# Kernel optimization log

Measured on AMD Instinct MI355X. Metric: run time of the kernel, lower is better.

## Reference

```python
import jax, jax.numpy as jnp
import numpy as np

N = 100000   # nodes
E = 1600000  # edges (avg degree 16)
D = 64       # feature dim
H = 256      # MLP hidden
EPS = 0.0    # init_eps, learn_eps=False


def setup_inputs() -> dict:
    key = jax.random.key(0)
    k = jax.random.split(key, 5)
    feat = jax.random.normal(k[0], (N, D), dtype=jnp.float32)
    W1 = jax.random.normal(k[1], (D, H), dtype=jnp.float32) / np.sqrt(D)
    b1 = jnp.zeros((H,), dtype=jnp.float32)
    W2 = jax.random.normal(k[2], (H, D), dtype=jnp.float32) / np.sqrt(H)
    b2 = jnp.zeros((D,), dtype=jnp.float32)
    src = jax.random.randint(k[3], (E,), 0, N, dtype=jnp.int32)
    dst = jax.random.randint(k[4], (E,), 0, N, dtype=jnp.int32)
    return {"feat": feat, "W1": W1, "b1": b1, "W2": W2, "b2": b2,
            "src": src, "dst": dst}


def reference(feat, W1, b1, W2, b2, src, dst):
    # message: m_e = feat[src_e]; reduce: sum over edges into dst
    neigh = jax.ops.segment_sum(feat[src], dst, num_segments=N)  # [N, D]
    # eps-scaled self loop (no edge features => feat_dst unpadded)
    rst = (1.0 + EPS) * feat + neigh
    # apply_func: 2-layer MLP with ReLU
    h = jax.nn.relu(rst @ W1 + b1)
    return h @ W2 + b2
```

## Files before the change

### kernel.cpp

```cpp
#include <hip/hip_runtime.h>

#define D 64
#define H 256
#define SRC_MASK ((1u << 23) - 1)

#define NBF 512
#define NPBF 256
#define CAPF 4096
#define PJ 8

#define NB2 512
#define NPB2 256
#define CAP2 6144
#define PEPT 16

typedef __bf16 bf16x8 __attribute__((ext_vector_type(8)));
typedef float f32x16 __attribute__((ext_vector_type(16)));
typedef unsigned int uint4v __attribute__((ext_vector_type(4)));

__device__ inline unsigned pack_bf16x2(float a, float b) {
    unsigned short ua = __builtin_bit_cast(unsigned short, (__bf16)a);
    unsigned short ub = __builtin_bit_cast(unsigned short, (__bf16)b);
    return (unsigned)ua | ((unsigned)ub << 16);
}

__device__ inline void lane32_swap(unsigned x, unsigned y, unsigned& o0, unsigned& o1) {
#if __has_builtin(__builtin_amdgcn_permlane32_swap)
    typedef unsigned int uint2v __attribute__((ext_vector_type(2)));
    uint2v r = __builtin_amdgcn_permlane32_swap(x, y, false, false);
    o0 = r.x; o1 = r.y;
#else
    unsigned xs = __shfl_xor((int)x, 32, 64);
    unsigned ys = __shfl_xor((int)y, 32, 64);
    bool hi = (threadIdx.x & 32) != 0;
    o0 = hi ? ys : x;
    o1 = hi ? y : xs;
#endif
}

__device__ inline bf16x8 weight_frag(const float* __restrict__ W1,
                                     const float* __restrict__ W2,
                                     int fid, int lane) {
    int g = lane >> 5, c = lane & 31;
    bf16x8 v;
    if (fid < 32) {
        int ht = fid >> 2, ks = fid & 3;
        const float* col = W1 + (32 * ht + c);
        int k0 = 16 * ks + 8 * g;
#pragma unroll
        for (int j = 0; j < 8; ++j) v[j] = (__bf16)col[(size_t)(k0 + j) * H];
    } else {
        int f = fid - 32;
        int dt = f >> 4, ks = f & 15;
        const float* col = W2 + (32 * dt + c);
        int k0 = 16 * ks + 8 * g;
#pragma unroll
        for (int j = 0; j < 8; ++j) v[j] = (__bf16)col[(size_t)(k0 + j) * D];
    }
    return v;
}

__global__ __launch_bounds__(1024) void fused_front_kernel(
        const float* __restrict__ feat, unsigned short* __restrict__ featb,
        int n8v,
        const float* __restrict__ W1, const float* __restrict__ W2,
        bf16x8* __restrict__ wf,
        const int* __restrict__ src, const int* __restrict__ dst,
        int* __restrict__ cur,
        unsigned* __restrict__ packed, uint2* __restrict__ ovf,
        int E, int npb, int pB, int prepB) {
    int blk = blockIdx.x;
    int tid = threadIdx.x;

    if (blk >= pB + prepB) {
        int i = (blk - pB - prepB) * 1024 + tid;
        if (i < n8v) {
            const float4* f4 = reinterpret_cast<const float4*>(feat);
            float4 a = f4[2 * i];
            float4 b = f4[2 * i + 1];
            uint4v o = { pack_bf16x2(a.x, a.y), pack_bf16x2(a.z, a.w),
                         pack_bf16x2(b.x, b.y), pack_bf16x2(b.z, b.w) };
            reinterpret_cast<uint4v*>(featb)[i] = o;
        }
        return;
    }
    if (blk >= pB) {
        int fid = (blk - pB) * 16 + (tid >> 6);
        int lane = tid & 63;
        if (fid < 64) wf[fid * 64 + lane] = weight_frag(W1, W2, fid, lane);
        return;
    }

    __shared__ int cnt[NBF];
    __shared__ int resv[NBF];
    if (tid < NBF) cnt[tid] = 0;
    __syncthreads();
    int e0 = blk * (1024 * PJ);
    unsigned myP[PJ];
    int myB[PJ], myR[PJ];
#pragma unroll
    for (int j = 0; j < PJ; ++j) {
        int e = e0 + j * 1024 + tid;
        if (e < E) {
            int d = dst[e];
            int s = src[e];
            int b = (int)((unsigned)d / (unsigned)npb);
            myB[j] = b;
            myR[j] = atomicAdd(&cnt[b], 1);
            myP[j] = ((unsigned)(d - b * npb) << 23) | (unsigned)s;
        } else {
            myB[j] = -1;
        }
    }
    __syncthreads();
    if (tid < NBF && cnt[tid] > 0)
        resv[tid] = atomicAdd(&cur[tid], cnt[tid]);
    __syncthreads();
#pragma unroll
    for (int j = 0; j < PJ; ++j) {
        if (myB[j] < 0) continue;
        int slot = resv[myB[j]] + myR[j];
        if (slot < CAPF) {
            packed[(size_t)myB[j] * CAPF + slot] = myP[j];
        } else {
            int oi = atomicAdd(&cur[NBF], 1);
            ovf[oi] = make_uint2(((unsigned)myB[j] << 16) | (myP[j] >> 23),
                                 myP[j] & SRC_MASK);
        }
    }
}

__global__ __launch_bounds__(1024, 2) void csr_gather_fixed_kernel(
        const unsigned* __restrict__ packed, const int* __restrict__ cur,
        const uint2* __restrict__ ovf,
        const unsigned short* __restrict__ featb,
        unsigned short* __restrict__ rstb, int n, int npb) {
    __shared__ int hist[NPBF];
    __shared__ int start[NPBF];
    __shared__ int cursor[NPBF];
    __shared__ unsigned raw[CAPF];
    __shared__ int srt[CAPF];

    int b = blockIdx.x;
    int tid = threadIdx.x;
    int node0 = b * npb;

    if (tid < NPBF) hist[tid] = 0;
    __syncthreads();

    int stored = cur[b];
    if (stored > CAPF) stored = CAPF;
    int ovfn = cur[NBF];
    const unsigned* win = packed + (size_t)b * CAPF;

    for (int k = tid; k < stored; k += 1024) {
        unsigned p = __builtin_nontemporal_load(win + k);
        raw[k] = p;
        atomicAdd(&hist[p >> 23], 1);
    }
    __syncthreads();

    if (tid < NPBF) start[tid] = hist[tid];
    __syncthreads();
    for (int o = 1; o < NPBF; o <<= 1) {
        int t = (tid < NPBF && tid >= o) ? start[tid - o] : 0;
        __syncthreads();
        if (tid < NPBF) start[tid] += t;
        __syncthreads();
    }
    if (tid < NPBF) {
        int ex = start[tid] - hist[tid];
        start[tid] = ex;
        cursor[tid] = ex;
    }
    __syncthreads();

    for (int k = tid; k < stored; k += 1024) {
        unsigned p = raw[k];
        int pos = atomicAdd(&cursor[p >> 23], 1);
        srt[pos] = (int)(p & SRC_MASK);
    }
    __syncthreads();

    int g = tid & 7;
    const bf16x8* f8 = reinterpret_cast<const bf16x8*>(featb);
    for (int ln = tid >> 3; ln < npb; ln += 128) {
        int node = node0 + ln;
        if (node >= n) break;
        bf16x8 self = f8[node * 8 + g];
        float acc[8];
#pragma unroll
        for (int j = 0; j < 8; ++j) acc[j] = (float)self[j];

        int s0 = start[ln];
        int e1 = s0 + hist[ln];
        int i = s0;
        for (; i + 4 <= e1; i += 4) {
            int u0 = srt[i + 0];
            int u1 = srt[i + 1];
            int u2 = srt[i + 2];
            int u3 = srt[i + 3];
            bf16x8 v0 = f8[u0 * 8 + g];
            bf16x8 v1 = f8[u1 * 8 + g];
            bf16x8 v2 = f8[u2 * 8 + g];
            bf16x8 v3 = f8[u3 * 8 + g];
#pragma unroll
            for (int j = 0; j < 8; ++j)
                acc[j] += ((float)v0[j] + (float)v1[j]) +
                          ((float)v2[j] + (float)v3[j]);
        }
        for (; i < e1; ++i) {
            bf16x8 v = f8[srt[i] * 8 + g];
#pragma unroll
            for (int j = 0; j < 8; ++j) acc[j] += (float)v[j];
        }
        if (ovfn > 0) {
            unsigned key = ((unsigned)b << 16) | (unsigned)ln;
            for (int k = 0; k < ovfn; ++k) {
                uint2 oe = ovf[k];
                if (oe.x == key) {
                    bf16x8 v = f8[oe.y * 8 + g];
#pragma unroll
                    for (int j = 0; j < 8; ++j) acc[j] += (float)v[j];
                }
            }
        }

        uint4v o = { pack_bf16x2(acc[0], acc[1]), pack_bf16x2(acc[2], acc[3]),
                     pack_bf16x2(acc[4], acc[5]), pack_bf16x2(acc[6], acc[7]) };
        reinterpret_cast<uint4v*>(rstb)[node * 8 + g] = o;
    }
}

__global__ void prep_weights_kernel(const float* __restrict__ W1,
                                    const float* __restrict__ W2,
                                    bf16x8* __restrict__ wf,
                                    int* __restrict__ gz) {
    if (blockIdx.x >= 64) {
        for (int i = threadIdx.x; i < 2 * NB2; i += 64) gz[i] = 0;
        return;
    }
    wf[blockIdx.x * 64 + threadIdx.x] =
        weight_frag(W1, W2, blockIdx.x, threadIdx.x);
}

__global__ __launch_bounds__(256) void cvt_hist_kernel(
        const float* __restrict__ feat, unsigned short* __restrict__ featb,
        int n8, const int* __restrict__ dst, int E, int* __restrict__ gcnt,
        int npb, int nb, int cvtB) {
    int tid = threadIdx.x;
    if ((int)blockIdx.x < cvtB) {
        int i = blockIdx.x * 256 + tid;
        if (i < n8) {
            const float4* f4 = reinterpret_cast<const float4*>(feat);
            float4 a = f4[2 * i];
            float4 b = f4[2 * i + 1];
            uint4v o = { pack_bf16x2(a.x, a.y), pack_bf16x2(a.z, a.w),
                         pack_bf16x2(b.x, b.y), pack_bf16x2(b.z, b.w) };
            reinterpret_cast<uint4v*>(featb)[i] = o;
        }
    } else {
        __shared__ int c[NB2];
        for (int i = tid; i < NB2; i += 256) c[i] = 0;
        __syncthreads();
        int hb = gridDim.x - cvtB;
        for (int e = (blockIdx.x - cvtB) * 256 + tid; e < E; e += hb * 256)
            atomicAdd(&c[(unsigned)dst[e] / (unsigned)npb], 1);
        __syncthreads();
        for (int i = tid; i < nb; i += 256)
            if (c[i] > 0) atomicAdd(&gcnt[i], c[i]);
    }
}

__global__ __launch_bounds__(1024) void partition2_kernel(
        const int* __restrict__ src, const int* __restrict__ dst,
        const int* __restrict__ gcnt, int* __restrict__ cur2,
        unsigned* __restrict__ packed, int E, int npb, int nb) {
    __shared__ int sg[NB2];
    __shared__ int cnt[NB2];
    __shared__ int base_s[NB2];
    int tid = threadIdx.x;
    if (tid < NB2) {
        sg[tid] = (tid < nb) ? gcnt[tid] : 0;
        cnt[tid] = 0;
    }
    __syncthreads();
    for (int o = 1; o < NB2; o <<= 1) {
        int t = (tid < NB2 && tid >= o) ? sg[tid - o] : 0;
        __syncthreads();
        if (tid < NB2) sg[tid] += t;
        __syncthreads();
    }
    int e0 = blockIdx.x * (1024 * PEPT);
    unsigned myP[PEPT];
    int myB[PEPT], myR[PEPT];
#pragma unroll
    for (int j = 0; j < PEPT; ++j) {
        int e = e0 + j * 1024 + tid;
        if (e < E) {
            int d = dst[e];
            int s = src[e];
            int b = (unsigned)d / (unsigned)npb;
            myB[j] = b;
            myR[j] = atomicAdd(&cnt[b], 1);
            myP[j] = ((unsigned)(d - b * npb) << 23) | (unsigned)s;
        } else {
            myB[j] = -1;
        }
    }
    __syncthreads();
    if (tid < nb && cnt[tid] > 0)
        base_s[tid] = (sg[tid] - gcnt[tid]) + atomicAdd(&cur2[tid], cnt[tid]);
    __syncthreads();
#pragma unroll
    for (int j = 0; j < PEPT; ++j) {
        if (myB[j] >= 0) packed[base_s[myB[j]] + myR[j]] = myP[j];
    }
}

__global__ __launch_bounds__(1024, 2) void csr_gather2_kernel(
        const unsigned* __restrict__ packed, const int* __restrict__ gcnt,
        const unsigned short* __restrict__ featb,
        int* __restrict__ csr_g, unsigned short* __restrict__ rstb,
        int n, int npb, int nb) {
    __shared__ int sg[NB2];
    __shared__ int hist[NPB2];
    __shared__ int start[NPB2];
    __shared__ int cursor[NPB2];
    __shared__ unsigned raw[CAP2];
    __shared__ int srt[CAP2];

    int b = blockIdx.x;
    int tid = threadIdx.x;
    int node0 = b * npb;

    if (tid < NB2) sg[tid] = (tid < nb) ? gcnt[tid] : 0;
    if (tid < NPB2) hist[tid] = 0;
    __syncthreads();
    for (int o = 1; o < NB2; o <<= 1) {
        int t = (tid < NB2 && tid >= o) ? sg[tid - o] : 0;
        __syncthreads();
        if (tid < NB2) sg[tid] += t;
        __syncthreads();
    }
    int ie = sg[b];
    int ib = (b > 0) ? sg[b - 1] : 0;
    bool useG = (ie - ib) > CAP2;

    for (int k = ib + tid; k < ie; k += 1024) {
        unsigned p = packed[k];
        if (!useG) raw[k - ib] = p;
        atomicAdd(&hist[p >> 23], 1);
    }
    __syncthreads();

    if (tid < NPB2) start[tid] = hist[tid];
    __syncthreads();
    for (int o = 1; o < NPB2; o <<= 1) {
        int t = (tid < NPB2 && tid >= o) ? start[tid - o] : 0;
        __syncthreads();
        if (tid < NPB2) start[tid] += t;
        __syncthreads();
    }
    if (tid < NPB2) {
        int excl = start[tid] - hist[tid];
        start[tid] = excl;
        cursor[tid] = excl;
    }
    __syncthreads();

    int cnt_e = ie - ib;
    if (!useG) {
        for (int k = tid; k < cnt_e; k += 1024) {
            unsigned p = raw[k];
            int pos = atomicAdd(&cursor[p >> 23], 1);
            srt[pos] = (int)(p & SRC_MASK);
        }
    } else {
        for (int k = ib + tid; k < ie; k += 1024) {
            unsigned p = packed[k];
            int pos = atomicAdd(&cursor[p >> 23], 1);
            csr_g[ib + pos] = (int)(p & SRC_MASK);
        }
    }
    __syncthreads();

    int g = tid & 7;
    const bf16x8* f8 = reinterpret_cast<const bf16x8*>(featb);
    for (int ln = tid >> 3; ln < npb; ln += 128) {
        int node = node0 + ln;
        if (node >= n) break;
        bf16x8 self = f8[node * 8 + g];
        float acc[8];
#pragma unroll
        for (int j = 0; j < 8; ++j) acc[j] = (float)self[j];

        int s0 = start[ln];
        int e1 = s0 + hist[ln];
        const int* lst = useG ? (csr_g + ib) : srt;
        int i = s0;
        for (; i + 4 <= e1; i += 4) {
            int u0 = lst[i + 0];
            int u1 = lst[i + 1];
            int u2 = lst[i + 2];
            int u3 = lst[i + 3];
            bf16x8 v0 = f8[u0 * 8 + g];
            bf16x8 v1 = f8[u1 * 8 + g];
            bf16x8 v2 = f8[u2 * 8 + g];
            bf16x8 v3 = f8[u3 * 8 + g];
#pragma unroll
            for (int j = 0; j < 8; ++j)
                acc[j] += ((float)v0[j] + (float)v1[j]) +
                          ((float)v2[j] + (float)v3[j]);
        }
        for (; i < e1; ++i) {
            bf16x8 v = f8[lst[i] * 8 + g];
#pragma unroll
            for (int j = 0; j < 8; ++j) acc[j] += (float)v[j];
        }

        uint4v o = { pack_bf16x2(acc[0], acc[1]), pack_bf16x2(acc[2], acc[3]),
                     pack_bf16x2(acc[4], acc[5]), pack_bf16x2(acc[6], acc[7]) };
        reinterpret_cast<uint4v*>(rstb)[node * 8 + g] = o;
    }
}

template <bool BF16>
__global__ __launch_bounds__(512, 4) void mlp_mfma_kernel(
        const void* __restrict__ rstv, const bf16x8* __restrict__ wf,
        const float* __restrict__ b1, const float* __restrict__ b2,
        float* __restrict__ out, int n, int ntiles) {
    __shared__ bf16x8 swf[64 * 64];
    __shared__ float sb1[H];
    __shared__ float sb2[D];

    for (int i = threadIdx.x; i < 64 * 64; i += 512) swf[i] = wf[i];
    if (threadIdx.x < H) sb1[threadIdx.x] = b1[threadIdx.x];
    if (threadIdx.x < D) sb2[threadIdx.x] = b2[threadIdx.x];
    __syncthreads();

    int lane = threadIdx.x & 63;
    int wid  = threadIdx.x >> 6;
    int g = lane >> 5, c = lane & 31;

    int tile = blockIdx.x * 8 + wid;
    if (tile >= ntiles) return;
    int node = tile * 32 + c;
    bool valid = node < n;
    int nodeC = valid ? node : (n - 1);

    bf16x8 bfr[4];
    if constexpr (BF16) {
        const bf16x8* rb = reinterpret_cast<const bf16x8*>(rstv) +
                           (size_t)nodeC * 8 + g;
#pragma unroll
        for (int ks = 0; ks < 4; ++ks) bfr[ks] = rb[2 * ks];
    } else {
        const float* rrow = reinterpret_cast<const float*>(rstv) +
                            (size_t)nodeC * D + 8 * g;
#pragma unroll
        for (int ks = 0; ks < 4; ++ks) {
            float4 lo = *reinterpret_cast<const float4*>(rrow + 16 * ks);
            float4 hi = *reinterpret_cast<const float4*>(rrow + 16 * ks + 4);
            bf16x8 v;
            v[0] = (__bf16)lo.x; v[1] = (__bf16)lo.y; v[2] = (__bf16)lo.z; v[3] = (__bf16)lo.w;
            v[4] = (__bf16)hi.x; v[5] = (__bf16)hi.y; v[6] = (__bf16)hi.z; v[7] = (__bf16)hi.w;
            bfr[ks] = v;
        }
    }

    f32x16 acc2_0 = {};
    f32x16 acc2_1 = {};

#pragma unroll
    for (int ht = 0; ht < 8; ++ht) {
        f32x16 a1 = {};
#pragma unroll
        for (int ks = 0; ks < 4; ++ks)
            a1 = __builtin_amdgcn_mfma_f32_32x32x16_bf16(
                     swf[(ht * 4 + ks) * 64 + lane], bfr[ks], a1, 0, 0, 0);

        float hv[16];
#pragma unroll
        for (int q = 0; q < 4; ++q) {
            float4 bq = *reinterpret_cast<const float4*>(&sb1[32 * ht + 8 * q + 4 * g]);
            hv[4 * q + 0] = fmaxf(a1[4 * q + 0] + bq.x, 0.0f);
            hv[4 * q + 1] = fmaxf(a1[4 * q + 1] + bq.y, 0.0f);
            hv[4 * q + 2] = fmaxf(a1[4 * q + 2] + bq.z, 0.0f);
            hv[4 * q + 3] = fmaxf(a1[4 * q + 3] + bq.w, 0.0f);
        }

#pragma unroll
        for (int half = 0; half < 2; ++half) {
            const float* hs = hv + 8 * half;
            unsigned plo0 = pack_bf16x2(hs[0], hs[1]);
            unsigned plo1 = pack_bf16x2(hs[2], hs[3]);
            unsigned phi0 = pack_bf16x2(hs[4], hs[5]);
            unsigned phi1 = pack_bf16x2(hs[6], hs[7]);
            unsigned f0, f2, f1, f3;
            lane32_swap(plo0, phi0, f0, f2);
            lane32_swap(plo1, phi1, f1, f3);
            uint4v fr = { f0, f1, f2, f3 };
            bf16x8 b2f = __builtin_bit_cast(bf16x8, fr);
            int ks2 = 2 * ht + half;
            acc2_0 = __builtin_amdgcn_mfma_f32_32x32x16_bf16(
                         swf[(32 + 0 * 16 + ks2) * 64 + lane], b2f, acc2_0, 0, 0, 0);
            acc2_1 = __builtin_amdgcn_mfma_f32_32x32x16_bf16(
                         swf[(32 + 1 * 16 + ks2) * 64 + lane], b2f, acc2_1, 0, 0, 0);
        }
    }

    if (!valid) return;
    float* orow = out + (size_t)node * D;
#pragma unroll
    for (int dt = 0; dt < 2; ++dt) {
        const f32x16& a = dt ? acc2_1 : acc2_0;
#pragma unroll
        for (int q = 0; q < 4; ++q) {
            int d0 = 32 * dt + 8 * q + 4 * g;
            float4 bq = *reinterpret_cast<const float4*>(&sb2[d0]);
            float4 v;
            v.x = a[4 * q + 0] + bq.x;
            v.y = a[4 * q + 1] + bq.y;
            v.z = a[4 * q + 2] + bq.z;
            v.w = a[4 * q + 3] + bq.w;
            *reinterpret_cast<float4*>(orow + d0) = v;
        }
    }
}

__global__ void copy_feat_kernel(const float* __restrict__ feat,
                                 float* __restrict__ rst, int n4) {
    int i = blockIdx.x * blockDim.x + threadIdx.x;
    if (i < n4) {
        reinterpret_cast<float4*>(rst)[i] =
            reinterpret_cast<const float4*>(feat)[i];
    }
}

__global__ void scatter_add_kernel(const float* __restrict__ feat,
                                   const int* __restrict__ src,
                                   const int* __restrict__ dst,
                                   float* rst, int E) {
    int gid = blockIdx.x * blockDim.x + threadIdx.x;
    int e = gid >> 4;
    if (e >= E) return;
    int d4 = (gid & 15) << 2;
    int s = src[e];
    int t = dst[e];
    float4 v = *reinterpret_cast<const float4*>(&feat[s * D + d4]);
    float* p = &rst[t * D + d4];
    atomicAdd(p + 0, v.x);
    atomicAdd(p + 1, v.y);
    atomicAdd(p + 2, v.z);
    atomicAdd(p + 3, v.w);
}

__global__ __launch_bounds__(512) void mlp_valu_kernel(
        const float* rst,
        const float* __restrict__ W1, const float* __restrict__ b1,
        const float* __restrict__ W2, const float* __restrict__ b2,
        float* out, int n) {
    __shared__ float sW1t[H * D];
    __shared__ float sW2 [H * D];
    __shared__ float sb1[H];
    __shared__ float sb2[D];

    for (int i = threadIdx.x; i < D * H; i += 512) {
        int d = i >> 8;
        int j = i & (H - 1);
        sW1t[j * D + d] = W1[i];
        sW2[i] = W2[i];
    }
    if (threadIdx.x < H) sb1[threadIdx.x] = b1[threadIdx.x];
    if (threadIdx.x < D) sb2[threadIdx.x] = b2[threadIdx.x];
    __syncthreads();

    int node = blockIdx.x * 512 + threadIdx.x;
    if (node >= n) return;

    float x[D];
    const float4* xr = reinterpret_cast<const float4*>(&rst[node * D]);
#pragma unroll
    for (int d4 = 0; d4 < D / 4; ++d4) {
        float4 v = xr[d4];
        x[d4 * 4 + 0] = v.x; x[d4 * 4 + 1] = v.y;
        x[d4 * 4 + 2] = v.z; x[d4 * 4 + 3] = v.w;
    }
    float acc[D];
#pragma unroll
    for (int d = 0; d < D; ++d) acc[d] = sb2[d];
    for (int j = 0; j < H; ++j) {
        float h = sb1[j];
        const float4* w1 = reinterpret_cast<const float4*>(&sW1t[j * D]);
#pragma unroll
        for (int d4 = 0; d4 < D / 4; ++d4) {
            float4 w = w1[d4];
            h += x[d4 * 4 + 0] * w.x + x[d4 * 4 + 1] * w.y +
                 x[d4 * 4 + 2] * w.z + x[d4 * 4 + 3] * w.w;
        }
        h = fmaxf(h, 0.0f);
        const float4* w2 = reinterpret_cast<const float4*>(&sW2[j * D]);
#pragma unroll
        for (int d4 = 0; d4 < D / 4; ++d4) {
            float4 w = w2[d4];
            acc[d4 * 4 + 0] += h * w.x; acc[d4 * 4 + 1] += h * w.y;
            acc[d4 * 4 + 2] += h * w.z; acc[d4 * 4 + 3] += h * w.w;
        }
    }
    float4* op = reinterpret_cast<float4*>(&out[node * D]);
#pragma unroll
    for (int d4 = 0; d4 < D / 4; ++d4) {
        float4 v;
        v.x = acc[d4 * 4 + 0]; v.y = acc[d4 * 4 + 1];
        v.z = acc[d4 * 4 + 2]; v.w = acc[d4 * 4 + 3];
        op[d4] = v;
    }
}

extern "C" void kernel_launch(void* const* d_in, const int* in_sizes, int n_in,
                              void* d_out, int out_size, void* d_ws, size_t ws_size,
                              hipStream_t stream) {
    const float* feat = (const float*)d_in[0];
    const float* W1   = (const float*)d_in[1];
    const float* b1   = (const float*)d_in[2];
    const float* W2   = (const float*)d_in[3];
    const float* b2   = (const float*)d_in[4];
    const int*   src  = (const int*)d_in[5];
    const int*   dst  = (const int*)d_in[6];
    float* buf = (float*)d_out;

    int n = in_sizes[0] / D;
    int E = in_sizes[5];
    char* ws = (char*)d_ws;

    int npbF = (n + NBF - 1) / NBF;
    int nbF  = (n + npbF - 1) / npbF;
    size_t o1 = 0;
    auto a1 = [&](size_t bytes) { size_t c = o1; o1 = (o1 + bytes + 255) & ~(size_t)255; return c; };
    size_t t1_wf     = a1(64 * 64 * sizeof(bf16x8));
    size_t t1_ctrl   = a1((NBF + 1) * sizeof(int));
    size_t t1_packed = a1((size_t)NBF * CAPF * sizeof(unsigned));
    size_t t1_ovf    = a1((size_t)E * sizeof(uint2));
    size_t t1_featb  = a1((size_t)n * D * 2);
    size_t t1_rstb   = a1((size_t)n * D * 2);
    size_t need1 = o1;
    bool tier1 = (npbF <= NPBF) && (ws_size >= need1);

    if (tier1) {
        bf16x8*   wf     = (bf16x8*)(ws + t1_wf);
        int*      ctrl   = (int*)(ws + t1_ctrl);
        unsigned* packed = (unsigned*)(ws + t1_packed);
        uint2*    ovf    = (uint2*)(ws + t1_ovf);
        unsigned short* featb = (unsigned short*)(ws + t1_featb);
        unsigned short* rstb  = (unsigned short*)(ws + t1_rstb);

        hipMemsetAsync(ctrl, 0, (NBF + 1) * sizeof(int), stream);

        int n8v  = n * D / 8;
        int cvtB = (n8v + 1023) / 1024;
        int pB   = (E + 1024 * PJ - 1) / (1024 * PJ);
        int prepB = 4;
        fused_front_kernel<<<pB + prepB + cvtB, 1024, 0, stream>>>(
            feat, featb, n8v, W1, W2, wf, src, dst, ctrl, packed, ovf,
            E, npbF, pB, prepB);

        csr_gather_fixed_kernel<<<nbF, 1024, 0, stream>>>(
            packed, ctrl, ovf, featb, rstb, n, npbF);

        int ntiles = (n + 31) / 32;
        mlp_mfma_kernel<true><<<(ntiles + 7) / 8, 512, 0, stream>>>(
            rstb, wf, b1, b2, buf, n, ntiles);
        return;
    }

    int npb2 = (n + NB2 - 1) / NB2;
    int nb2  = (n + npb2 - 1) / npb2;
    size_t o2 = 0;
    auto a2 = [&](size_t bytes) { size_t c = o2; o2 = (o2 + bytes + 255) & ~(size_t)255; return c; };
    size_t t2_wf     = a2(64 * 64 * sizeof(bf16x8));
    size_t t2_gcnt   = a2(2 * NB2 * sizeof(int));
    size_t t2_packed = a2((size_t)E * sizeof(unsigned));
    size_t t2_csrg   = a2((size_t)E * sizeof(int));
    size_t t2_featb  = a2((size_t)n * D * 2);
    size_t t2_rstb   = a2((size_t)n * D * 2);
    size_t need2 = o2;
    bool haveWf = ws_size >= 64 * 64 * sizeof(bf16x8);
    bool tier2  = (npb2 <= NPB2) && (n < (1 << 23)) && (ws_size >= need2);

    if (tier2) {
        bf16x8*   wf     = (bf16x8*)(ws + t2_wf);
        int*      gcnt   = (int*)(ws + t2_gcnt);
        int*      cur2   = gcnt + NB2;
        unsigned* packed = (unsigned*)(ws + t2_packed);
        int*      csr_g  = (int*)(ws + t2_csrg);
        unsigned short* featb = (unsigned short*)(ws + t2_featb);
        unsigned short* rstb  = (unsigned short*)(ws + t2_rstb);

        prep_weights_kernel<<<65, 64, 0, stream>>>(W1, W2, wf, gcnt);

        int n8   = n * D / 8;
        int cvtB = (n8 + 255) / 256;
        cvt_hist_kernel<<<cvtB + 784, 256, 0, stream>>>(
            feat, featb, n8, dst, E, gcnt, npb2, nb2, cvtB);

        int pB2 = (E + 1024 * PEPT - 1) / (1024 * PEPT);
        partition2_kernel<<<pB2, 1024, 0, stream>>>(
            src, dst, gcnt, cur2, packed, E, npb2, nb2);

        csr_gather2_kernel<<<nb2, 1024, 0, stream>>>(
            packed, gcnt, featb, csr_g, rstb, n, npb2, nb2);

        int ntiles = (n + 31) / 32;
        mlp_mfma_kernel<true><<<(ntiles + 7) / 8, 512, 0, stream>>>(
            rstb, wf, b1, b2, buf, n, ntiles);
        return;
    }

    if (haveWf) {
        bf16x8* wf = (bf16x8*)ws;
        prep_weights_kernel<<<64, 64, 0, stream>>>(W1, W2, wf, (int*)ws);
        int n4 = n * D / 4;
        copy_feat_kernel<<<(n4 + 255) / 256, 256, 0, stream>>>(feat, buf, n4);
        int threads = E * 16;
        scatter_add_kernel<<<(threads + 255) / 256, 256, 0, stream>>>(
            feat, src, dst, buf, E);
        int ntiles = (n + 31) / 32;
        mlp_mfma_kernel<false><<<(ntiles + 7) / 8, 512, 0, stream>>>(
            buf, wf, b1, b2, buf, n, ntiles);
    } else {
        int n4 = n * D / 4;
        copy_feat_kernel<<<(n4 + 255) / 256, 256, 0, stream>>>(feat, buf, n4);
        int threads = E * 16;
        scatter_add_kernel<<<(threads + 255) / 256, 256, 0, stream>>>(
            feat, src, dst, buf, E);
        mlp_valu_kernel<<<(n + 511) / 512, 512, 0, stream>>>(
            buf, W1, b1, W2, b2, buf, n);
    }
}
```

Before: 75.77 us.

## Fuse neighbor gather with MFMA MLP in one kernel via LDS staging

Merges the CSR gather kernel and the MLP kernel on the tier-1 path. Each block writes its aggregated bf16 rows into XOR-swizzled LDS, then loads the weights into LDS and runs the two-layer MFMA MLP directly on them. This removes the rstb global round trip and one kernel launch. In exchange, LDS use per block grows by roughly 96KB, which limits occupancy. The MLP phase also uses only 8 of 16 waves, and the weights are reloaded once per block (512 blocks).

```diff
diff --git a/kernel.cpp b/kernel.cpp
--- a/kernel.cpp
+++ b/kernel.cpp
@@ -130,16 +130,22 @@
     }
 }
 
-__global__ __launch_bounds__(1024, 2) void csr_gather_fixed_kernel(
+__global__ __launch_bounds__(1024, 4) void csr_gather_mlp_kernel(
         const unsigned* __restrict__ packed, const int* __restrict__ cur,
         const uint2* __restrict__ ovf,
         const unsigned short* __restrict__ featb,
-        unsigned short* __restrict__ rstb, int n, int npb) {
+        const bf16x8* __restrict__ wf,
+        const float* __restrict__ b1, const float* __restrict__ b2,
+        float* __restrict__ out, int n, int npb) {
     __shared__ int hist[NPBF];
     __shared__ int start[NPBF];
     __shared__ int cursor[NPBF];
     __shared__ unsigned raw[CAPF];
     __shared__ int srt[CAPF];
+    __shared__ bf16x8 rstl[NPBF * 8];
+    __shared__ bf16x8 swf[64 * 64];
+    __shared__ float sb1[H];
+    __shared__ float sb2[D];
 
     int b = blockIdx.x;
     int tid = threadIdx.x;
@@ -182,292 +188,81 @@
     }
     __syncthreads();
 
-    int g = tid & 7;
-    const bf16x8* f8 = reinterpret_cast<const bf16x8*>(featb);
-    for (int ln = tid >> 3; ln < npb; ln += 128) {
-        int node = node0 + ln;
-        if (node >= n) break;
-        bf16x8 self = f8[node * 8 + g];
-        float acc[8];
-#pragma unroll
-        for (int j = 0; j < 8; ++j) acc[j] = (float)self[j];
-
-        int s0 = start[ln];
-        int e1 = s0 + hist[ln];
-        int i = s0;
-        for (; i + 4 <= e1; i += 4) {
-            int u0 = srt[i + 0];
-            int u1 = srt[i + 1];
-            int u2 = srt[i + 2];
-            int u3 = srt[i + 3];
-            bf16x8 v0 = f8[u0 * 8 + g];
-            bf16x8 v1 = f8[u1 * 8 + g];
-            bf16x8 v2 = f8[u2 * 8 + g];
-            bf16x8 v3 = f8[u3 * 8 + g];
-#pragma unroll
-            for (int j = 0; j < 8; ++j)
-                acc[j] += ((float)v0[j] + (float)v1[j]) +
-                          ((float)v2[j] + (float)v3[j]);
-        }
-        for (; i < e1; ++i) {
-            bf16x8 v = f8[srt[i] * 8 + g];
-#pragma unroll
-            for (int j = 0; j < 8; ++j) acc[j] += (float)v[j];
-        }
-        if (ovfn > 0) {
-            unsigned key = ((unsigned)b << 16) | (unsigned)ln;
-            for (int k = 0; k < ovfn; ++k) {
-                uint2 oe = ovf[k];
-                if (oe.x == key) {
-                    bf16x8 v = f8[oe.y * 8 + g];
-#pragma unroll
-                    for (int j = 0; j < 8; ++j) acc[j] += (float)v[j];
+    {
+        int g = tid & 7;
+        const bf16x8* f8 = reinterpret_cast<const bf16x8*>(featb);
+        for (int ln = tid >> 3; ln < npb; ln += 128) {
+            int node = node0 + ln;
+            int slot = ln * 8 + (g ^ (ln & 7));
+            if (node >= n) {
+                bf16x8 z = {};
+                rstl[slot] = z;
+                continue;
+            }
+            bf16x8 self = f8[node * 8 + g];
+            float acc[8];
+#pragma unroll
+            for (int j = 0; j < 8; ++j) acc[j] = (float)self[j];
+
+            int s0 = start[ln];
+            int e1 = s0 + hist[ln];
+            int i = s0;
+            for (; i + 4 <= e1; i += 4) {
+                int u0 = srt[i + 0];
+                int u1 = srt[i + 1];
+                int u2 = srt[i + 2];
+                int u3 = srt[i + 3];
+                bf16x8 v0 = f8[u0 * 8 + g];
+                bf16x8 v1 = f8[u1 * 8 + g];
+                bf16x8 v2 = f8[u2 * 8 + g];
+                bf16x8 v3 = f8[u3 * 8 + g];
+#pragma unroll
+                for (int j = 0; j < 8; ++j)
+                    acc[j] += ((float)v0[j] + (float)v1[j]) +
+                              ((float)v2[j] + (float)v3[j]);
+            }
+            for (; i < e1; ++i) {
+                bf16x8 v = f8[srt[i] * 8 + g];
+#pragma unroll
+                for (int j = 0; j < 8; ++j) acc[j] += (float)v[j];
+            }
+            if (ovfn > 0) {
+                unsigned key = ((unsigned)b << 16) | (unsigned)ln;
+                for (int k = 0; k < ovfn; ++k) {
+                    uint2 oe = ovf[k];
+                    if (oe.x == key) {
+                        bf16x8 v = f8[oe.y * 8 + g];
+#pragma unroll
+                        for (int j = 0; j < 8; ++j) acc[j] += (float)v[j];
+                    }
                 }
             }
-        }
-
-        uint4v o = { pack_bf16x2(acc[0], acc[1]), pack_bf16x2(acc[2], acc[3]),
-                     pack_bf16x2(acc[4], acc[5]), pack_bf16x2(acc[6], acc[7]) };
-        reinterpret_cast<uint4v*>(rstb)[node * 8 + g] = o;
-    }
-}
-
-__global__ void prep_weights_kernel(const float* __restrict__ W1,
-                                    const float* __restrict__ W2,
-                                    bf16x8* __restrict__ wf,
-                                    int* __restrict__ gz) {
-    if (blockIdx.x >= 64) {
-        for (int i = threadIdx.x; i < 2 * NB2; i += 64) gz[i] = 0;
-        return;
-    }
-    wf[blockIdx.x * 64 + threadIdx.x] =
-        weight_frag(W1, W2, blockIdx.x, threadIdx.x);
-}
-
-__global__ __launch_bounds__(256) void cvt_hist_kernel(
-        const float* __restrict__ feat, unsigned short* __restrict__ featb,
-        int n8, const int* __restrict__ dst, int E, int* __restrict__ gcnt,
-        int npb, int nb, int cvtB) {
-    int tid = threadIdx.x;
-    if ((int)blockIdx.x < cvtB) {
-        int i = blockIdx.x * 256 + tid;
-        if (i < n8) {
-            const float4* f4 = reinterpret_cast<const float4*>(feat);
-            float4 a = f4[2 * i];
-            float4 b = f4[2 * i + 1];
-            uint4v o = { pack_bf16x2(a.x, a.y), pack_bf16x2(a.z, a.w),
-                         pack_bf16x2(b.x, b.y), pack_bf16x2(b.z, b.w) };
-            reinterpret_cast<uint4v*>(featb)[i] = o;
-        }
-    } else {
-        __shared__ int c[NB2];
-        for (int i = tid; i < NB2; i += 256) c[i] = 0;
-        __syncthreads();
-        int hb = gridDim.x - cvtB;
-        for (int e = (blockIdx.x - cvtB) * 256 + tid; e < E; e += hb * 256)
-            atomicAdd(&c[(unsigned)dst[e] / (unsigned)npb], 1);
-        __syncthreads();
-        for (int i = tid; i < nb; i += 256)
-            if (c[i] > 0) atomicAdd(&gcnt[i], c[i]);
-    }
-}
-
-__global__ __launch_bounds__(1024) void partition2_kernel(
-        const int* __restrict__ src, const int* __restrict__ dst,
-        const int* __restrict__ gcnt, int* __restrict__ cur2,
-        unsigned* __restrict__ packed, int E, int npb, int nb) {
-    __shared__ int sg[NB2];
-    __shared__ int cnt[NB2];
-    __shared__ int base_s[NB2];
-    int tid = threadIdx.x;
-    if (tid < NB2) {
-        sg[tid] = (tid < nb) ? gcnt[tid] : 0;
-        cnt[tid] = 0;
-    }
-    __syncthreads();
-    for (int o = 1; o < NB2; o <<= 1) {
-        int t = (tid < NB2 && tid >= o) ? sg[tid - o] : 0;
-        __syncthreads();
-        if (tid < NB2) sg[tid] += t;
-        __syncthreads();
-    }
-    int e0 = blockIdx.x * (1024 * PEPT);
-    unsigned myP[PEPT];
-    int myB[PEPT], myR[PEPT];
-#pragma unroll
-    for (int j = 0; j < PEPT; ++j) {
-        int e = e0 + j * 1024 + tid;
-        if (e < E) {
-            int d = dst[e];
-            int s = src[e];
-            int b = (unsigned)d / (unsigned)npb;
-            myB[j] = b;
-            myR[j] = atomicAdd(&cnt[b], 1);
-            myP[j] = ((unsigned)(d - b * npb) << 23) | (unsigned)s;
-        } else {
-            myB[j] = -1;
-        }
-    }
-    __syncthreads();
-    if (tid < nb && cnt[tid] > 0)
-        base_s[tid] = (sg[tid] - gcnt[tid]) + atomicAdd(&cur2[tid], cnt[tid]);
-    __syncthreads();
-#pragma unroll
-    for (int j = 0; j < PEPT; ++j) {
-        if (myB[j] >= 0) packed[base_s[myB[j]] + myR[j]] = myP[j];
-    }
-}
-
-__global__ __launch_bounds__(1024, 2) void csr_gather2_kernel(
-        const unsigned* __restrict__ packed, const int* __restrict__ gcnt,
-        const unsigned short* __restrict__ featb,
-        int* __restrict__ csr_g, unsigned short* __restrict__ rstb,
-        int n, int npb, int nb) {
-    __shared__ int sg[NB2];
-    __shared__ int hist[NPB2];
-    __shared__ int start[NPB2];
-    __shared__ int cursor[NPB2];
-    __shared__ unsigned raw[CAP2];
-    __shared__ int srt[CAP2];
-
-    int b = blockIdx.x;
-    int tid = threadIdx.x;
-    int node0 = b * npb;
-
-    if (tid < NB2) sg[tid] = (tid < nb) ? gcnt[tid] : 0;
-    if (tid < NPB2) hist[tid] = 0;
-    __syncthreads();
-    for (int o = 1; o < NB2; o <<= 1) {
-        int t = (tid < NB2 && tid >= o) ? sg[tid - o] : 0;
-        __syncthreads();
-        if (tid < NB2) sg[tid] += t;
-        __syncthreads();
-    }
-    int ie = sg[b];
-    int ib = (b > 0) ? sg[b - 1] : 0;
-    bool useG = (ie - ib) > CAP2;
-
-    for (int k = ib + tid; k < ie; k += 1024) {
-        unsigned p = packed[k];
-        if (!useG) raw[k - ib] = p;
-        atomicAdd(&hist[p >> 23], 1);
-    }
-    __syncthreads();
-
-    if (tid < NPB2) start[tid] = hist[tid];
-    __syncthreads();
-    for (int o = 1; o < NPB2; o <<= 1) {
-        int t = (tid < NPB2 && tid >= o) ? start[tid - o] : 0;
-        __syncthreads();
-        if (tid < NPB2) start[tid] += t;
-        __syncthreads();
-    }
-    if (tid < NPB2) {
-        int excl = start[tid] - hist[tid];
-        start[tid] = excl;
-        cursor[tid] = excl;
-    }
-    __syncthreads();
-
-    int cnt_e = ie - ib;
-    if (!useG) {
-        for (int k = tid; k < cnt_e; k += 1024) {
-            unsigned p = raw[k];
-            int pos = atomicAdd(&cursor[p >> 23], 1);
-            srt[pos] = (int)(p & SRC_MASK);
-        }
-    } else {
-        for (int k = ib + tid; k < ie; k += 1024) {
-            unsigned p = packed[k];
-            int pos = atomicAdd(&cursor[p >> 23], 1);
-            csr_g[ib + pos] = (int)(p & SRC_MASK);
-        }
-    }
-    __syncthreads();
-
-    int g = tid & 7;
-    const bf16x8* f8 = reinterpret_cast<const bf16x8*>(featb);
-    for (int ln = tid >> 3; ln < npb; ln += 128) {
-        int node = node0 + ln;
-        if (node >= n) break;
-        bf16x8 self = f8[node * 8 + g];
-        float acc[8];
-#pragma unroll
-        for (int j = 0; j < 8; ++j) acc[j] = (float)self[j];
-
-        int s0 = start[ln];
-        int e1 = s0 + hist[ln];
-        const int* lst = useG ? (csr_g + ib) : srt;
-        int i = s0;
-        for (; i + 4 <= e1; i += 4) {
-            int u0 = lst[i + 0];
-            int u1 = lst[i + 1];
-            int u2 = lst[i + 2];
-            int u3 = lst[i + 3];
-            bf16x8 v0 = f8[u0 * 8 + g];
-            bf16x8 v1 = f8[u1 * 8 + g];
-            bf16x8 v2 = f8[u2 * 8 + g];
-            bf16x8 v3 = f8[u3 * 8 + g];
-#pragma unroll
-            for (int j = 0; j < 8; ++j)
-                acc[j] += ((float)v0[j] + (float)v1[j]) +
-                          ((float)v2[j] + (float)v3[j]);
-        }
-        for (; i < e1; ++i) {
-            bf16x8 v = f8[lst[i] * 8 + g];
-#pragma unroll
-            for (int j = 0; j < 8; ++j) acc[j] += (float)v[j];
-        }
-
-        uint4v o = { pack_bf16x2(acc[0], acc[1]), pack_bf16x2(acc[2], acc[3]),
-                     pack_bf16x2(acc[4], acc[5]), pack_bf16x2(acc[6], acc[7]) };
-        reinterpret_cast<uint4v*>(rstb)[node * 8 + g] = o;
-    }
-}
-
-template <bool BF16>
-__global__ __launch_bounds__(512, 4) void mlp_mfma_kernel(
-        const void* __restrict__ rstv, const bf16x8* __restrict__ wf,
-        const float* __restrict__ b1, const float* __restrict__ b2,
-        float* __restrict__ out, int n, int ntiles) {
-    __shared__ bf16x8 swf[64 * 64];
-    __shared__ float sb1[H];
-    __shared__ float sb2[D];
-
-    for (int i = threadIdx.x; i < 64 * 64; i += 512) swf[i] = wf[i];
-    if (threadIdx.x < H) sb1[threadIdx.x] = b1[threadIdx.x];
-    if (threadIdx.x < D) sb2[threadIdx.x] = b2[threadIdx.x];
-    __syncthreads();
-
-    int lane = threadIdx.x & 63;
-    int wid  = threadIdx.x >> 6;
-    int g = lane >> 5, c = lane & 31;
-
-    int tile = blockIdx.x * 8 + wid;
-    if (tile >= ntiles) return;
-    int node = tile * 32 + c;
-    bool valid = node < n;
-    int nodeC = valid ? node : (n - 1);
+
+            uint4v o = { pack_bf16x2(acc[0], acc[1]), pack_bf16x2(acc[2], acc[3]),
+                         pack_bf16x2(acc[4], acc[5]), pack_bf16x2(acc[6], acc[7]) };
+            rstl[slot] = __builtin_bit_cast(bf16x8, o);
+        }
+    }
+    __syncthreads();
+
+    for (int i = tid; i < 64 * 64; i += 1024) swf[i] = wf[i];
+    if (tid < H) sb1[tid] = b1[tid];
+    if (tid < D) sb2[tid] = b2[tid];
+    __syncthreads();
+
+    int lane = tid & 63;
+    int w = tid >> 6;
+    int tiles = (npb + 31) >> 5;
+    if (w >= tiles) return;
+    int c = lane & 31, g2 = lane >> 5;
+    int r = 32 * w + c;
+    int node = node0 + r;
+    bool valid = (r < npb) && (node < n);
 
     bf16x8 bfr[4];
-    if constexpr (BF16) {
-        const bf16x8* rb = reinterpret_cast<const bf16x8*>(rstv) +
-                           (size_t)nodeC * 8 + g;
-#pragma unroll
-        for (int ks = 0; ks < 4; ++ks) bfr[ks] = rb[2 * ks];
-    } else {
-        const float* rrow = reinterpret_cast<const float*>(rstv) +
-                            (size_t)nodeC * D + 8 * g;
-#pragma unroll
-        for (int ks = 0; ks < 4; ++ks) {
-            float4 lo = *reinterpret_cast<const float4*>(rrow + 16 * ks);
-            float4 hi = *reinterpret_cast<const float4*>(rrow + 16 * ks + 4);
-            bf16x8 v;
-            v[0] = (__bf16)lo.x; v[1] = (__bf16)lo.y; v[2] = (__bf16)lo.z; v[3] = (__bf16)lo.w;
-            v[4] = (__bf16)hi.x; v[5] = (__bf16)hi.y; v[6] = (__bf16)hi.z; v[7] = (__bf16)hi.w;
-            bfr[ks] = v;
-        }
-    }
+#pragma unroll
+    for (int ks = 0; ks < 4; ++ks)
+        bfr[ks] = rstl[r * 8 + ((2 * ks + g2) ^ (r & 7))];
 
     f32x16 acc2_0 = {};
     f32x16 acc2_1 = {};
@@ -483,7 +278,7 @@
         float hv[16];
 #pragma unroll
         for (int q = 0; q < 4; ++q) {
-            float4 bq = *reinterpret_cast<const float4*>(&sb1[32 * ht + 8 * q + 4 * g]);
+            float4 bq = *reinterpret_cast<const float4*>(&sb1[32 * ht + 8 * q + 4 * g2]);
             hv[4 * q + 0] = fmaxf(a1[4 * q + 0] + bq.x, 0.0f);
             hv[4 * q + 1] = fmaxf(a1[4 * q + 1] + bq.y, 0.0f);
             hv[4 * q + 2] = fmaxf(a1[4 * q + 2] + bq.z, 0.0f);
@@ -517,6 +312,303 @@
         const f32x16& a = dt ? acc2_1 : acc2_0;
 #pragma unroll
         for (int q = 0; q < 4; ++q) {
+            int d0 = 32 * dt + 8 * q + 4 * g2;
+            float4 bq = *reinterpret_cast<const float4*>(&sb2[d0]);
+            float4 v;
+            v.x = a[4 * q + 0] + bq.x;
+            v.y = a[4 * q + 1] + bq.y;
+            v.z = a[4 * q + 2] + bq.z;
+            v.w = a[4 * q + 3] + bq.w;
+            *reinterpret_cast<float4*>(orow + d0) = v;
+        }
+    }
+}
+
+__global__ void prep_weights_kernel(const float* __restrict__ W1,
+                                    const float* __restrict__ W2,
+                                    bf16x8* __restrict__ wf,
+                                    int* __restrict__ gz) {
+    if (blockIdx.x >= 64) {
+        for (int i = threadIdx.x; i < 2 * NB2; i += 64) gz[i] = 0;
+        return;
+    }
+    wf[blockIdx.x * 64 + threadIdx.x] =
+        weight_frag(W1, W2, blockIdx.x, threadIdx.x);
+}
+
+__global__ __launch_bounds__(256) void cvt_hist_kernel(
+        const float* __restrict__ feat, unsigned short* __restrict__ featb,
+        int n8, const int* __restrict__ dst, int E, int* __restrict__ gcnt,
+        int npb, int nb, int cvtB) {
+    int tid = threadIdx.x;
+    if ((int)blockIdx.x < cvtB) {
+        int i = blockIdx.x * 256 + tid;
+        if (i < n8) {
+            const float4* f4 = reinterpret_cast<const float4*>(feat);
+            float4 a = f4[2 * i];
+            float4 b = f4[2 * i + 1];
+            uint4v o = { pack_bf16x2(a.x, a.y), pack_bf16x2(a.z, a.w),
+                         pack_bf16x2(b.x, b.y), pack_bf16x2(b.z, b.w) };
+            reinterpret_cast<uint4v*>(featb)[i] = o;
+        }
+    } else {
+        __shared__ int c[NB2];
+        for (int i = tid; i < NB2; i += 256) c[i] = 0;
+        __syncthreads();
+        int hb = gridDim.x - cvtB;
+        for (int e = (blockIdx.x - cvtB) * 256 + tid; e < E; e += hb * 256)
+            atomicAdd(&c[(unsigned)dst[e] / (unsigned)npb], 1);
+        __syncthreads();
+        for (int i = tid; i < nb; i += 256)
+            if (c[i] > 0) atomicAdd(&gcnt[i], c[i]);
+    }
+}
+
+__global__ __launch_bounds__(1024) void partition2_kernel(
+        const int* __restrict__ src, const int* __restrict__ dst,
+        const int* __restrict__ gcnt, int* __restrict__ cur2,
+        unsigned* __restrict__ packed, int E, int npb, int nb) {
+    __shared__ int sg[NB2];
+    __shared__ int cnt[NB2];
+    __shared__ int base_s[NB2];
+    int tid = threadIdx.x;
+    if (tid < NB2) {
+        sg[tid] = (tid < nb) ? gcnt[tid] : 0;
+        cnt[tid] = 0;
+    }
+    __syncthreads();
+    for (int o = 1; o < NB2; o <<= 1) {
+        int t = (tid < NB2 && tid >= o) ? sg[tid - o] : 0;
+        __syncthreads();
+        if (tid < NB2) sg[tid] += t;
+        __syncthreads();
+    }
+    int e0 = blockIdx.x * (1024 * PEPT);
+    unsigned myP[PEPT];
+    int myB[PEPT], myR[PEPT];
+#pragma unroll
+    for (int j = 0; j < PEPT; ++j) {
+        int e = e0 + j * 1024 + tid;
+        if (e < E) {
+            int d = dst[e];
+            int s = src[e];
+            int b = (unsigned)d / (unsigned)npb;
+            myB[j] = b;
+            myR[j] = atomicAdd(&cnt[b], 1);
+            myP[j] = ((unsigned)(d - b * npb) << 23) | (unsigned)s;
+        } else {
+            myB[j] = -1;
+        }
+    }
+    __syncthreads();
+    if (tid < nb && cnt[tid] > 0)
+        base_s[tid] = (sg[tid] - gcnt[tid]) + atomicAdd(&cur2[tid], cnt[tid]);
+    __syncthreads();
+#pragma unroll
+    for (int j = 0; j < PEPT; ++j) {
+        if (myB[j] >= 0) packed[base_s[myB[j]] + myR[j]] = myP[j];
+    }
+}
+
+__global__ __launch_bounds__(1024, 2) void csr_gather2_kernel(
+        const unsigned* __restrict__ packed, const int* __restrict__ gcnt,
+        const unsigned short* __restrict__ featb,
+        int* __restrict__ csr_g, unsigned short* __restrict__ rstb,
+        int n, int npb, int nb) {
+    __shared__ int sg[NB2];
+    __shared__ int hist[NPB2];
+    __shared__ int start[NPB2];
+    __shared__ int cursor[NPB2];
+    __shared__ unsigned raw[CAP2];
+    __shared__ int srt[CAP2];
+
+    int b = blockIdx.x;
+    int tid = threadIdx.x;
+    int node0 = b * npb;
+
+    if (tid < NB2) sg[tid] = (tid < nb) ? gcnt[tid] : 0;
+    if (tid < NPB2) hist[tid] = 0;
+    __syncthreads();
+    for (int o = 1; o < NB2; o <<= 1) {
+        int t = (tid < NB2 && tid >= o) ? sg[tid - o] : 0;
+        __syncthreads();
+        if (tid < NB2) sg[tid] += t;
+        __syncthreads();
+    }
+    int ie = sg[b];
+    int ib = (b > 0) ? sg[b - 1] : 0;
+    bool useG = (ie - ib) > CAP2;
+
+    for (int k = ib + tid; k < ie; k += 1024) {
+        unsigned p = packed[k];
+        if (!useG) raw[k - ib] = p;
+        atomicAdd(&hist[p >> 23], 1);
+    }
+    __syncthreads();
+
+    if (tid < NPB2) start[tid] = hist[tid];
+    __syncthreads();
+    for (int o = 1; o < NPB2; o <<= 1) {
+        int t = (tid < NPB2 && tid >= o) ? start[tid - o] : 0;
+        __syncthreads();
+        if (tid < NPB2) start[tid] += t;
+        __syncthreads();
+    }
+    if (tid < NPB2) {
+        int excl = start[tid] - hist[tid];
+        start[tid] = excl;
+        cursor[tid] = excl;
+    }
+    __syncthreads();
+
+    int cnt_e = ie - ib;
+    if (!useG) {
+        for (int k = tid; k < cnt_e; k += 1024) {
+            unsigned p = raw[k];
+            int pos = atomicAdd(&cursor[p >> 23], 1);
+            srt[pos] = (int)(p & SRC_MASK);
+        }
+    } else {
+        for (int k = ib + tid; k < ie; k += 1024) {
+            unsigned p = packed[k];
+            int pos = atomicAdd(&cursor[p >> 23], 1);
+            csr_g[ib + pos] = (int)(p & SRC_MASK);
+        }
+    }
+    __syncthreads();
+
+    int g = tid & 7;
+    const bf16x8* f8 = reinterpret_cast<const bf16x8*>(featb);
+    for (int ln = tid >> 3; ln < npb; ln += 128) {
+        int node = node0 + ln;
+        if (node >= n) break;
+        bf16x8 self = f8[node * 8 + g];
+        float acc[8];
+#pragma unroll
+        for (int j = 0; j < 8; ++j) acc[j] = (float)self[j];
+
+        int s0 = start[ln];
+        int e1 = s0 + hist[ln];
+        const int* lst = useG ? (csr_g + ib) : srt;
+        int i = s0;
+        for (; i + 4 <= e1; i += 4) {
+            int u0 = lst[i + 0];
+            int u1 = lst[i + 1];
+            int u2 = lst[i + 2];
+            int u3 = lst[i + 3];
+            bf16x8 v0 = f8[u0 * 8 + g];
+            bf16x8 v1 = f8[u1 * 8 + g];
+            bf16x8 v2 = f8[u2 * 8 + g];
+            bf16x8 v3 = f8[u3 * 8 + g];
+#pragma unroll
+            for (int j = 0; j < 8; ++j)
+                acc[j] += ((float)v0[j] + (float)v1[j]) +
+                          ((float)v2[j] + (float)v3[j]);
+        }
+        for (; i < e1; ++i) {
+            bf16x8 v = f8[lst[i] * 8 + g];
+#pragma unroll
+            for (int j = 0; j < 8; ++j) acc[j] += (float)v[j];
+        }
+
+        uint4v o = { pack_bf16x2(acc[0], acc[1]), pack_bf16x2(acc[2], acc[3]),
+                     pack_bf16x2(acc[4], acc[5]), pack_bf16x2(acc[6], acc[7]) };
+        reinterpret_cast<uint4v*>(rstb)[node * 8 + g] = o;
+    }
+}
+
+template <bool BF16>
+__global__ __launch_bounds__(512, 4) void mlp_mfma_kernel(
+        const void* __restrict__ rstv, const bf16x8* __restrict__ wf,
+        const float* __restrict__ b1, const float* __restrict__ b2,
+        float* __restrict__ out, int n, int ntiles) {
+    __shared__ bf16x8 swf[64 * 64];
+    __shared__ float sb1[H];
+    __shared__ float sb2[D];
+
+    for (int i = threadIdx.x; i < 64 * 64; i += 512) swf[i] = wf[i];
+    if (threadIdx.x < H) sb1[threadIdx.x] = b1[threadIdx.x];
+    if (threadIdx.x < D) sb2[threadIdx.x] = b2[threadIdx.x];
+    __syncthreads();
+
+    int lane = threadIdx.x & 63;
+    int wid  = threadIdx.x >> 6;
+    int g = lane >> 5, c = lane & 31;
+
+    int tile = blockIdx.x * 8 + wid;
+    if (tile >= ntiles) return;
+    int node = tile * 32 + c;
+    bool valid = node < n;
+    int nodeC = valid ? node : (n - 1);
+
+    bf16x8 bfr[4];
+    if constexpr (BF16) {
+        const bf16x8* rb = reinterpret_cast<const bf16x8*>(rstv) +
+                           (size_t)nodeC * 8 + g;
+#pragma unroll
+        for (int ks = 0; ks < 4; ++ks) bfr[ks] = rb[2 * ks];
+    } else {
+        const float* rrow = reinterpret_cast<const float*>(rstv) +
+                            (size_t)nodeC * D + 8 * g;
+#pragma unroll
+        for (int ks = 0; ks < 4; ++ks) {
+            float4 lo = *reinterpret_cast<const float4*>(rrow + 16 * ks);
+            float4 hi = *reinterpret_cast<const float4*>(rrow + 16 * ks + 4);
+            bf16x8 v;
+            v[0] = (__bf16)lo.x; v[1] = (__bf16)lo.y; v[2] = (__bf16)lo.z; v[3] = (__bf16)lo.w;
+            v[4] = (__bf16)hi.x; v[5] = (__bf16)hi.y; v[6] = (__bf16)hi.z; v[7] = (__bf16)hi.w;
+            bfr[ks] = v;
+        }
+    }
+
+    f32x16 acc2_0 = {};
+    f32x16 acc2_1 = {};
+
+#pragma unroll
+    for (int ht = 0; ht < 8; ++ht) {
+        f32x16 a1 = {};
+#pragma unroll
+        for (int ks = 0; ks < 4; ++ks)
+            a1 = __builtin_amdgcn_mfma_f32_32x32x16_bf16(
+                     swf[(ht * 4 + ks) * 64 + lane], bfr[ks], a1, 0, 0, 0);
+
+        float hv[16];
+#pragma unroll
+        for (int q = 0; q < 4; ++q) {
+            float4 bq = *reinterpret_cast<const float4*>(&sb1[32 * ht + 8 * q + 4 * g]);
+            hv[4 * q + 0] = fmaxf(a1[4 * q + 0] + bq.x, 0.0f);
+            hv[4 * q + 1] = fmaxf(a1[4 * q + 1] + bq.y, 0.0f);
+            hv[4 * q + 2] = fmaxf(a1[4 * q + 2] + bq.z, 0.0f);
+            hv[4 * q + 3] = fmaxf(a1[4 * q + 3] + bq.w, 0.0f);
+        }
+
+#pragma unroll
+        for (int half = 0; half < 2; ++half) {
+            const float* hs = hv + 8 * half;
+            unsigned plo0 = pack_bf16x2(hs[0], hs[1]);
+            unsigned plo1 = pack_bf16x2(hs[2], hs[3]);
+            unsigned phi0 = pack_bf16x2(hs[4], hs[5]);
+            unsigned phi1 = pack_bf16x2(hs[6], hs[7]);
+            unsigned f0, f2, f1, f3;
+            lane32_swap(plo0, phi0, f0, f2);
+            lane32_swap(plo1, phi1, f1, f3);
+            uint4v fr = { f0, f1, f2, f3 };
+            bf16x8 b2f = __builtin_bit_cast(bf16x8, fr);
+            int ks2 = 2 * ht + half;
+            acc2_0 = __builtin_amdgcn_mfma_f32_32x32x16_bf16(
+                         swf[(32 + 0 * 16 + ks2) * 64 + lane], b2f, acc2_0, 0, 0, 0);
+            acc2_1 = __builtin_amdgcn_mfma_f32_32x32x16_bf16(
+                         swf[(32 + 1 * 16 + ks2) * 64 + lane], b2f, acc2_1, 0, 0, 0);
+        }
+    }
+
+    if (!valid) return;
+    float* orow = out + (size_t)node * D;
+#pragma unroll
+    for (int dt = 0; dt < 2; ++dt) {
+        const f32x16& a = dt ? acc2_1 : acc2_0;
+#pragma unroll
+        for (int q = 0; q < 4; ++q) {
             int d0 = 32 * dt + 8 * q + 4 * g;
             float4 bq = *reinterpret_cast<const float4*>(&sb2[d0]);
             float4 v;
@@ -643,7 +735,6 @@
     size_t t1_packed = a1((size_t)NBF * CAPF * sizeof(unsigned));
     size_t t1_ovf    = a1((size_t)E * sizeof(uint2));
     size_t t1_featb  = a1((size_t)n * D * 2);
-    size_t t1_rstb   = a1((size_t)n * D * 2);
     size_t need1 = o1;
     bool tier1 = (npbF <= NPBF) && (ws_size >= need1);
 
@@ -653,7 +744,6 @@
         unsigned* packed = (unsigned*)(ws + t1_packed);
         uint2*    ovf    = (uint2*)(ws + t1_ovf);
         unsigned short* featb = (unsigned short*)(ws + t1_featb);
-        unsigned short* rstb  = (unsigned short*)(ws + t1_rstb);
 
         hipMemsetAsync(ctrl, 0, (NBF + 1) * sizeof(int), stream);
 
@@ -665,12 +755,8 @@
             feat, featb, n8v, W1, W2, wf, src, dst, ctrl, packed, ovf,
             E, npbF, pB, prepB);
 
-        csr_gather_fixed_kernel<<<nbF, 1024, 0, stream>>>(
-            packed, ctrl, ovf, featb, rstb, n, npbF);
-
-        int ntiles = (n + 31) / 32;
-        mlp_mfma_kernel<true><<<(ntiles + 7) / 8, 512, 0, stream>>>(
-            rstb, wf, b1, b2, buf, n, ntiles);
+        csr_gather_mlp_kernel<<<nbF, 1024, 0, stream>>>(
+            packed, ctrl, ovf, featb, wf, b1, b2, buf, n, npbF);
         return;
     }
 
```

After: 80.76 us. +6.6%, slower.
